# Optimization experiments

Measured on AMD Instinct MI355X. Metric: run time of the kernel, lower is better.

Reference implementation:

```python
import jax, jax.numpy as jnp
import numpy as np
from jax import lax

_CLIP_MIN = 1e-06
_CLIP_MAX = 1.0
_POS_ALPHA = 0.0005
NUM_CLASSES = 21
RADIUS = 3
HALF_D = RADIUS * RADIUS
POOL = 3
PAD = POOL // 2
IGNORE = 255
LAM = 0.5  # loss_weight_lambda, lambda_way=1


def _max_pool(x):
    # NCHW max pool, kernel=stride=3, padding=1
    return lax.reduce_window(x, -jnp.inf, lax.max,
                             (1, 1, POOL, POOL), (1, 1, POOL, POOL),
                             ((0, 0), (0, 0), (PAD, PAD), (PAD, PAD)))


def _get_pairs(x):
    # stack radius*radius shifted crops -> [N, C, r^2, nh, nw]
    h, w = x.shape[2], x.shape[3]
    nh, nw = h - RADIUS + 1, w - RADIUS + 1
    crops = [x[:, :, y:y + nh, xo:xo + nw] for y in range(RADIUS) for xo in range(RADIUS)]
    return jnp.stack(crops, axis=2)


def _log_det_by_cholesky(m):
    chol = jnp.linalg.cholesky(m)
    return 2.0 * jnp.sum(jnp.log(jnp.diagonal(chol, axis1=-2, axis2=-1) + 1e-08), axis=-1)


def _rmi_lower_bound(labels_4d, probs_4d):
    la = _max_pool(labels_4d)
    pr = _max_pool(probs_4d)
    n, c = la.shape[0], la.shape[1]
    la_v = _get_pairs(la).reshape(n, c, HALF_D, -1)   # [N,C,d,L]
    pr_v = _get_pairs(pr).reshape(n, c, HALF_D, -1)
    la_v = la_v - jnp.mean(la_v, axis=3, keepdims=True)
    pr_v = pr_v - jnp.mean(pr_v, axis=3, keepdims=True)
    la_cov = jnp.einsum('ncdl,ncel->ncde', la_v, la_v)
    pr_cov = jnp.einsum('ncdl,ncel->ncde', pr_v, pr_v)
    eye = jnp.eye(HALF_D, dtype=la_cov.dtype)
    pr_cov_inv = jnp.linalg.inv(pr_cov + eye * _POS_ALPHA)
    la_pr_cov = jnp.einsum('ncdl,ncel->ncde', la_v, pr_v)
    appro_var = la_cov - jnp.einsum('ncde,ncef,ncgf->ncdg', la_pr_cov, pr_cov_inv, la_pr_cov)
    rmi_now = 0.5 * _log_det_by_cholesky(appro_var + eye * _POS_ALPHA)  # [N,C]
    rmi_per_class = jnp.mean(rmi_now.reshape(-1, NUM_CLASSES), axis=0) / float(HALF_D)
    return jnp.sum(rmi_per_class)


def setup_inputs() -> dict:
    key = jax.random.key(0)
    k1, k2 = jax.random.split(key)
    score = jax.random.normal(k1, (4, NUM_CLASSES, 512, 512), dtype=jnp.float32)
    target = jax.random.randint(k2, (4, 512, 512), 0, NUM_CLASSES, dtype=jnp.int64)
    return {"score": score, "target": target}


def reference(score, target):
    # cross entropy with ignore_index=255, mean reduction
    logp = jax.nn.log_softmax(score, axis=1)                      # [N,C,H,W]
    valid_ce = (target != IGNORE)
    safe_t = jnp.where(valid_ce, target, 0)
    nll = -jnp.take_along_axis(logp, safe_t[:, None].astype(jnp.int32), axis=1)[:, 0]
    normal_loss = jnp.sum(jnp.where(valid_ce, nll, 0.0)) / jnp.sum(valid_ce.astype(jnp.float32))

    # valid one-hot labels and masked sigmoid probs
    mask = (target < NUM_CLASSES)                                 # [N,H,W]
    maskf = mask.astype(jnp.float32)
    onehot = jax.nn.one_hot((target * mask).astype(jnp.int32), NUM_CLASSES, dtype=jnp.float32)
    onehot = onehot * maskf[..., None]                            # [N,H,W,C]
    onehot = jnp.transpose(onehot, (0, 3, 1, 2))                  # [N,C,H,W]
    probs = jnp.clip(jax.nn.sigmoid(score) * maskf[:, None], _CLIP_MIN, _CLIP_MAX)

    rmi_loss = _rmi_lower_bound(onehot, probs)
    return LAM * normal_loss + rmi_loss * (1.0 - LAM)
```

## Files before the change

kernel.cpp:

```cpp
#include <hip/hip_runtime.h>
#include <cfloat>
#include <cmath>

#define DEVINL __device__ __forceinline__

constexpr int N_ = 4, C_ = 21, H_ = 512, W_ = 512;
constexpr int P_ = 171;
constexpr int Q_ = 169;
constexpr int NC_ = N_ * C_;
constexpr int HW_ = H_ * W_;
constexpr int PP_ = 29241;
constexpr int PROW_ = 172;
constexpr int PPAD_ = PROW_ * P_;
constexpr int NCOV_ = 189;
constexpr float EPS_ = 5e-4f;
constexpr int RC_ = 29;
constexpr int G_ = 43;

constexpr int NB_CE = N_ * HW_ / 4 / 256;
constexpr int NB_PL = (NC_ * P_ * G_ + 255) / 256;

DEVINL constexpr int tstart(int d) { return d * 9 - d * (d - 1) / 2; }

DEVINL float wave_sum(float v) {
#pragma unroll
    for (int o = 32; o > 0; o >>= 1) v += __shfl_down(v, o, 64);
    return v;
}

__global__ __launch_bounds__(256) void k_bits(const int* __restrict__ target,
                                              unsigned* __restrict__ pack) {
    int tid = blockIdx.x * 256 + threadIdx.x;
    if (tid >= N_ * PP_) return;
    int cell = tid % PP_;
    int n = tid / PP_;
    int j = cell % P_;
    int i = cell / P_;
    int hl = 3 * i - 1; if (hl < 0) hl = 0;
    int wl = 3 * j - 1; if (wl < 0) wl = 0;
    int hmax = 3 * i + 1, wmax = 3 * j + 1;
    const int* tb = target + (size_t)n * HW_;
    unsigned oh = 0, px = 0;
#pragma unroll
    for (int r = 0; r < 3; ++r) {
        int hh = hl + r;
        bool hv = hh <= hmax;
        const int* trow = tb + hh * W_;
#pragma unroll
        for (int dc = 0; dc < 3; ++dc) {
            int ww = wl + dc;
            int t = trow[ww];
            if (hv && (ww <= wmax) && t >= 0 && t < C_) {
                oh |= 1u << t;
                px |= 1u << (r * 3 + dc);
            }
        }
    }
    pack[tid] = oh | (px << 23);
}

template <int IDX>
DEVINL void do_cell(const float (&f)[3][16], unsigned pk, int c, float* prp, float* lap) {
    unsigned px = pk >> 23;
    float vm = -FLT_MAX;
#pragma unroll
    for (int r = 0; r < 3; ++r)
#pragma unroll
        for (int dc = 0; dc < 3; ++dc)
            vm = fmaxf(vm, ((px >> (r * 3 + dc)) & 1u) ? f[r][IDX + dc] : -FLT_MAX);
    float p = __builtin_amdgcn_rcpf(1.f + __expf(-vm));
    p = fminf(fmaxf(p, 1e-6f), 1.f);
    *prp = p;
    *lap = ((pk >> c) & 1u) ? 1.f : 0.f;
}

__global__ __launch_bounds__(256) void k_mix(const float* __restrict__ score,
                                             const int* __restrict__ target,
                                             const unsigned* __restrict__ pack,
                                             float* __restrict__ pr,
                                             float* __restrict__ la,
                                             float* __restrict__ cov) {
    int bid = blockIdx.x;
    int t = threadIdx.x;

    if (bid < NB_CE) {
        __shared__ float rn[4], rc[4];
        int tid = bid * 256 + t;
        int p0 = tid * 4;
        int n = p0 >> 18;
        int hw = p0 & (HW_ - 1);
        const float* sp = score + (size_t)n * C_ * HW_ + hw;
        int4 t4 = *(const int4*)(target + p0);

        float4 se = {0.f, 0.f, 0.f, 0.f};
        float4 stgt = {0.f, 0.f, 0.f, 0.f};
        float4 s[7];
#pragma unroll
        for (int cb = 0; cb < C_; cb += 7) {
#pragma unroll
            for (int u = 0; u < 7; ++u)
                s[u] = *(const float4*)(sp + (size_t)(cb + u) * HW_);
            __builtin_amdgcn_sched_barrier(0);
#pragma unroll
            for (int u = 0; u < 7; ++u) {
                int c = cb + u;
                se.x += __expf(s[u].x);
                se.y += __expf(s[u].y);
                se.z += __expf(s[u].z);
                se.w += __expf(s[u].w);
                if (t4.x == c) stgt.x = s[u].x;
                if (t4.y == c) stgt.y = s[u].y;
                if (t4.z == c) stgt.z = s[u].z;
                if (t4.w == c) stgt.w = s[u].w;
            }
        }
        float nll = 0.f, cnt = 0.f;
        if (t4.x != 255) { nll += __logf(se.x) - stgt.x; cnt += 1.f; }
        if (t4.y != 255) { nll += __logf(se.y) - stgt.y; cnt += 1.f; }
        if (t4.z != 255) { nll += __logf(se.z) - stgt.z; cnt += 1.f; }
        if (t4.w != 255) { nll += __logf(se.w) - stgt.w; cnt += 1.f; }

        nll = wave_sum(nll);
        cnt = wave_sum(cnt);
        int wv = t >> 6, lane = t & 63;
        if (lane == 0) { rn[wv] = nll; rc[wv] = cnt; }
        __syncthreads();
        if (t == 0)
            atomicAdd(&cov[NC_ * NCOV_ + 0], rn[0] + rn[1] + rn[2] + rn[3]);
        if (t == 64)
            atomicAdd(&cov[NC_ * NCOV_ + 1], rc[0] + rc[1] + rc[2] + rc[3]);
    } else {
        int tid = (bid - NB_CE) * 256 + t;
        if (tid >= NC_ * P_ * G_) return;
        int g = tid % G_;
        int rest = tid / G_;
        int i = rest % P_;
        int ncidx = rest / P_;
        int n = ncidx / C_;
        int c = ncidx - n * C_;

        int hl = 3 * i - 1; if (hl < 0) hl = 0;
        int b = (g == 0) ? 0 : 12 * g - 4;
        int o3 = (b + 15 < W_) ? 12 : 8;

        const float* sb = score + (size_t)ncidx * HW_ + (size_t)hl * W_ + b;
        float f[3][16];
#pragma unroll
        for (int r = 0; r < 3; ++r) {
            const float* rp = sb + r * W_;
            float4 q0 = *(const float4*)(rp);
            float4 q1 = *(const float4*)(rp + 4);
            float4 q2 = *(const float4*)(rp + 8);
            float4 q3 = *(const float4*)(rp + o3);
            f[r][0] = q0.x;  f[r][1] = q0.y;  f[r][2] = q0.z;  f[r][3] = q0.w;
            f[r][4] = q1.x;  f[r][5] = q1.y;  f[r][6] = q1.z;  f[r][7] = q1.w;
            f[r][8] = q2.x;  f[r][9] = q2.y;  f[r][10] = q2.z; f[r][11] = q2.w;
            f[r][12] = q3.x; f[r][13] = q3.y; f[r][14] = q3.z; f[r][15] = q3.w;
        }

        const unsigned* pkp = pack + n * PP_ + i * P_ + 4 * g;
        size_t ob = (size_t)ncidx * PPAD_ + (size_t)i * PROW_ + 4 * g;
        if (g == 0) {
            do_cell<0>(f, pkp[0], c, pr + ob + 0, la + ob + 0);
            do_cell<2>(f, pkp[1], c, pr + ob + 1, la + ob + 1);
            do_cell<5>(f, pkp[2], c, pr + ob + 2, la + ob + 2);
            do_cell<8>(f, pkp[3], c, pr + ob + 3, la + ob + 3);
        } else {
            do_cell<3>(f, pkp[0], c, pr + ob + 0, la + ob + 0);
            do_cell<6>(f, pkp[1], c, pr + ob + 1, la + ob + 1);
            do_cell<9>(f, pkp[2], c, pr + ob + 2, la + ob + 2);
            if (4 * g + 3 < P_)
                do_cell<12>(f, pkp[3], c, pr + ob + 3, la + ob + 3);
        }
    }
}

template <bool WITH_S1, int D0, int D1>
DEVINL void cov_tri(const float* __restrict__ X, float* __restrict__ cov,
                    int nc, int r0, int rend, int s1base, int s2base,
                    int tid, float (*red)[33]) {
    constexpr int NS2 = ((9 - D0) * (10 - D0) - (9 - D1) * (10 - D1)) / 2;
    constexpr int RLO = D0 / 3;
    constexpr int NS1 = WITH_S1 ? 9 : 0;
    constexpr int KOFF = tstart(D0);
    float s1[9], s2[NS2];
#pragma unroll
    for (int k = 0; k < 9; ++k) s1[k] = 0.f;
#pragma unroll
    for (int k = 0; k < NS2; ++k) s2[k] = 0.f;

    int nitems = (rend - r0) * G_;
    for (int idx = tid; idx < nitems; idx += 256) {
        int lr = idx / G_;
        int q = idx - lr * G_;
        int x0 = q * 4;
        const float* base = X + (size_t)(r0 + lr) * PROW_ + x0;
        float v[3][8];
#pragma unroll
        for (int r = RLO; r < 3; ++r) {
            float4 u0 = *(const float4*)(base + r * PROW_);
            float4 u1 = *(const float4*)(base + r * PROW_ + 4);
            v[r][0] = u0.x; v[r][1] = u0.y; v[r][2] = u0.z; v[r][3] = u0.w;
            v[r][4] = u1.x; v[r][5] = u1.y; v[r][6] = u1.z; v[r][7] = u1.w;
        }
#pragma unroll
        for (int p = 0; p < 4; ++p) {
            if (x0 + p < Q_) {
                if constexpr (WITH_S1) {
#pragma unroll
                    for (int d = 0; d < 9; ++d) s1[d] += v[d / 3][p + d % 3];
                }
                int k = 0;
#pragma unroll
                for (int d = D0; d < D1; ++d)
#pragma unroll
                    for (int e = d; e < 9; ++e) {
                        s2[k] += v[d / 3][p + d % 3] * v[e / 3][p + e % 3];
                        ++k;
                    }
            }
        }
    }

    int lane = tid & 63, wv = tid >> 6;
    if constexpr (WITH_S1) {
#pragma unroll
        for (int k = 0; k < 9; ++k) { float v2 = wave_sum(s1[k]); if (lane == 0) red[wv][k] = v2; }
    }
#pragma unroll
    for (int k = 0; k < NS2; ++k) { float v2 = wave_sum(s2[k]); if (lane == 0) red[wv][NS1 + k] = v2; }
    __syncthreads();
    for (int k = tid; k < NS1 + NS2; k += 256) {
        float v2 = red[0][k] + red[1][k] + red[2][k] + red[3][k];
        int dst = (WITH_S1 && k < 9) ? (s1base + k) : (s2base + KOFF + k - NS1);
        atomicAdd(&cov[nc * NCOV_ + dst], v2);
    }
}

template <int RA>
DEVINL void cov_ab(const float* __restrict__ A, const float* __restrict__ B,
                   float* __restrict__ cov, int nc, int r0, int rend,
                   int tid, float (*red)[33]) {
    float sab[27];
#pragma unroll
    for (int k = 0; k < 27; ++k) sab[k] = 0.f;

    int nitems = (rend - r0) * G_;
    for (int idx = tid; idx < nitems; idx += 256) {
        int lr = idx / G_;
        int q = idx - lr * G_;
        int x0 = q * 4;
        size_t off = (size_t)(r0 + lr) * PROW_ + x0;
        float a[8], b[3][8];
        {
            float4 u0 = *(const float4*)(A + off + RA * PROW_);
            float4 u1 = *(const float4*)(A + off + RA * PROW_ + 4);
            a[0] = u0.x; a[1] = u0.y; a[2] = u0.z; a[3] = u0.w;
            a[4] = u1.x; a[5] = u1.y; a[6] = u1.z; a[7] = u1.w;
        }
#pragma unroll
        for (int r = 0; r < 3; ++r) {
            float4 w0 = *(const float4*)(B + off + r * PROW_);
            float4 w1 = *(const float4*)(B + off + r * PROW_ + 4);
            b[r][0] = w0.x; b[r][1] = w0.y; b[r][2] = w0.z; b[r][3] = w0.w;
            b[r][4] = w1.x; b[r][5] = w1.y; b[r][6] = w1.z; b[r][7] = w1.w;
        }
#pragma unroll
        for (int p = 0; p < 4; ++p) {
            if (x0 + p < Q_) {
#pragma unroll
                for (int dm = 0; dm < 3; ++dm)
#pragma unroll
                    for (int e = 0; e < 9; ++e)
                        sab[dm * 9 + e] += a[p + dm] * b[e / 3][p + e % 3];
            }
        }
    }

    int lane = tid & 63, wv = tid >> 6;
#pragma unroll
    for (int k = 0; k < 27; ++k) { float v2 = wave_sum(sab[k]); if (lane == 0) red[wv][k] = v2; }
    __syncthreads();
    for (int k = tid; k < 27; k += 256) {
        float v2 = red[0][k] + red[1][k] + red[2][k] + red[3][k];
        atomicAdd(&cov[nc * NCOV_ + 108 + RA * 27 + k], v2);
    }
}

__global__ __launch_bounds__(256) void k_cov(const float* __restrict__ la,
                                             const float* __restrict__ pr,
                                             float* __restrict__ cov) {
    __shared__ float red[4][33];
    int nc = blockIdx.x;
    int chunk = blockIdx.y;
    int part = blockIdx.z;
    int r0 = chunk * RC_;
    int rend = r0 + RC_;
    if (rend > Q_) rend = Q_;
    int tid = threadIdx.x;
    const float* LA = la + (size_t)nc * PPAD_;
    const float* PR = pr + (size_t)nc * PPAD_;

    switch (part) {
        case 0: cov_tri<true, 0, 3>(LA, cov, nc, r0, rend, 0, 18, tid, red); break;
        case 1: cov_tri<false, 3, 9>(LA, cov, nc, r0, rend, 0, 18, tid, red); break;
        case 2: cov_tri<true, 0, 3>(PR, cov, nc, r0, rend, 9, 63, tid, red); break;
        case 3: cov_tri<false, 3, 9>(PR, cov, nc, r0, rend, 9, 63, tid, red); break;
        case 4: cov_ab<0>(LA, PR, cov, nc, r0, rend, tid, red); break;
        case 5: cov_ab<1>(LA, PR, cov, nc, r0, rend, tid, red); break;
        case 6: cov_ab<2>(LA, PR, cov, nc, r0, rend, tid, red); break;
    }
}

__global__ __launch_bounds__(128) void k_final(const float* __restrict__ cov,
                                               float* __restrict__ out) {
    __shared__ float red[128];
    int t = threadIdx.x;
    float my = 0.f;
    if (t < NC_) {
        const float* S = cov + t * NCOV_;
        const float Lf = (float)(Q_ * Q_);
        float sA[9], sB[9];
#pragma unroll
        for (int d = 0; d < 9; ++d) { sA[d] = S[d]; sB[d] = S[9 + d]; }
        float laC[45], M[45], Cm[81];
        {
            int k = 0;
#pragma unroll
            for (int d = 0; d < 9; ++d)
#pragma unroll
                for (int e = d; e < 9; ++e) {
                    laC[k] = S[18 + k] - sA[d] * sA[e] / Lf;
                    M[k] = S[63 + k] - sB[d] * sB[e] / Lf + (d == e ? EPS_ : 0.f);
                    ++k;
                }
#pragma unroll
            for (int d = 0; d < 9; ++d)
#pragma unroll
                for (int e = 0; e < 9; ++e)
                    Cm[d * 9 + e] = S[108 + d * 9 + e] - sA[d] * sB[e] / Lf;
        }
#pragma unroll
        for (int j = 0; j < 9; ++j) {
            float s = M[tstart(j)];
#pragma unroll
            for (int k = 0; k < j; ++k) { float l = M[tstart(k) + (j - k)]; s -= l * l; }
            float dj = sqrtf(fmaxf(s, 1e-30f));
            M[tstart(j)] = dj;
            float inv = 1.f / dj;
#pragma unroll
            for (int i = j + 1; i < 9; ++i) {
                float s2 = M[tstart(j) + (i - j)];
#pragma unroll
                for (int k = 0; k < j; ++k)
                    s2 -= M[tstart(k) + (i - k)] * M[tstart(k) + (j - k)];
                M[tstart(j) + (i - j)] = s2 * inv;
            }
        }
#pragma unroll
        for (int p = 0; p < 9; ++p) {
#pragma unroll
            for (int i = 0; i < 9; ++i) {
                float s = Cm[p * 9 + i];
#pragma unroll
                for (int k = 0; k < i; ++k)
                    s -= M[tstart(k) + (i - k)] * Cm[p * 9 + k];
                Cm[p * 9 + i] = s / M[tstart(i)];
            }
        }
#pragma unroll
        for (int d = 0; d < 9; ++d)
#pragma unroll
            for (int e = d; e < 9; ++e) {
                float s = 0.f;
#pragma unroll
                for (int i = 0; i < 9; ++i) s += Cm[d * 9 + i] * Cm[e * 9 + i];
                laC[tstart(d) + (e - d)] -= s;
                if (d == e) laC[tstart(d)] += EPS_;
            }
        float rmi = 0.f;
#pragma unroll
        for (int j = 0; j < 9; ++j) {
            float s = laC[tstart(j)];
#pragma unroll
            for (int k = 0; k < j; ++k) { float l = laC[tstart(k) + (j - k)]; s -= l * l; }
            float dj = sqrtf(fmaxf(s, 0.f));
            laC[tstart(j)] = dj;
            float inv = 1.f / fmaxf(dj, 1e-30f);
#pragma unroll
            for (int i = j + 1; i < 9; ++i) {
                float s2 = laC[tstart(j) + (i - j)];
#pragma unroll
                for (int k = 0; k < j; ++k)
                    s2 -= laC[tstart(k) + (i - k)] * laC[tstart(k) + (j - k)];
                laC[tstart(j) + (i - j)] = s2 * inv;
            }
            rmi += __logf(dj + 1e-8f);
        }
        my = rmi;
    }
    red[t] = my;
    __syncthreads();
#pragma unroll
    for (int o = 64; o > 0; o >>= 1) {
        if (t < o) red[t] += red[t + o];
        __syncthreads();
    }
    if (t == 0) {
        float rmi_total = red[0] / 36.f;
        float ce = cov[NC_ * NCOV_ + 0] / cov[NC_ * NCOV_ + 1];
        out[0] = 0.5f * ce + 0.5f * rmi_total;
    }
}

extern "C" void kernel_launch(void* const* d_in, const int* in_sizes, int n_in,
                              void* d_out, int out_size, void* d_ws, size_t ws_size,
                              hipStream_t stream) {
    const float* score = (const float*)d_in[0];
    const int* target = (const int*)d_in[1];
    float* pr = (float*)d_ws;
    float* la = pr + (size_t)NC_ * PPAD_;
    float* cov = la + (size_t)NC_ * PPAD_;
    unsigned* pack = (unsigned*)(cov + NC_ * NCOV_ + 2);
    hipMemsetAsync(cov, 0, (size_t)(NC_ * NCOV_ + 2) * sizeof(float), stream);

    k_bits<<<dim3((N_ * PP_ + 255) / 256), dim3(256), 0, stream>>>(target, pack);
    k_mix<<<dim3(NB_CE + NB_PL), dim3(256), 0, stream>>>(score, target, pack, pr, la, cov);
    k_cov<<<dim3(NC_, 6, 7), dim3(256), 0, stream>>>(la, pr, cov);
    k_final<<<dim3(1), dim3(128), 0, stream>>>(cov, (float*)d_out);
}
```

Baseline: 244.0 us.

## Stage covariance row window in LDS and compute all covariance parts per block

The covariance kernel used to launch seven separate blocks per (nc, chunk), each reading the same la/pr rows from global memory. Now one block per (nc, chunk) loads a 31-row window of la and pr into shared memory once, then runs both full triangular covariances and the three cross-covariance stages from LDS in sequence. This cuts redundant global reads and the launch to 504 blocks, at the cost of fewer blocks (lower parallelism) and more registers, since a full 45-entry triangle is now accumulated per thread. It also swaps a sched_barrier in the CE path for an empty asm register fence to pin the loads before use.

New measurement: 268.1 us. 9.9% more time.

```diff
diff --git a/kernel.cpp b/kernel.cpp
--- a/kernel.cpp
+++ b/kernel.cpp
@@ -16,9 +16,12 @@
 constexpr float EPS_ = 5e-4f;
 constexpr int RC_ = 29;
 constexpr int G_ = 43;
+constexpr int NWINMAX_ = 31;
 
 constexpr int NB_CE = N_ * HW_ / 4 / 256;
 constexpr int NB_PL = (NC_ * P_ * G_ + 255) / 256;
+
+typedef float f4_t __attribute__((ext_vector_type(4)));
 
 DEVINL constexpr int tstart(int d) { return d * 9 - d * (d - 1) / 2; }
 
@@ -94,13 +97,14 @@
 
         float4 se = {0.f, 0.f, 0.f, 0.f};
         float4 stgt = {0.f, 0.f, 0.f, 0.f};
-        float4 s[7];
+        f4_t s[7];
 #pragma unroll
         for (int cb = 0; cb < C_; cb += 7) {
 #pragma unroll
             for (int u = 0; u < 7; ++u)
-                s[u] = *(const float4*)(sp + (size_t)(cb + u) * HW_);
-            __builtin_amdgcn_sched_barrier(0);
+                s[u] = *(const f4_t*)(sp + (size_t)(cb + u) * HW_);
+            asm volatile("" : "+v"(s[0]), "+v"(s[1]), "+v"(s[2]), "+v"(s[3]),
+                              "+v"(s[4]), "+v"(s[5]), "+v"(s[6]));
 #pragma unroll
             for (int u = 0; u < 7; ++u) {
                 int c = cb + u;
@@ -175,29 +179,24 @@
     }
 }
 
-template <bool WITH_S1, int D0, int D1>
-DEVINL void cov_tri(const float* __restrict__ X, float* __restrict__ cov,
-                    int nc, int r0, int rend, int s1base, int s2base,
-                    int tid, float (*red)[33]) {
-    constexpr int NS2 = ((9 - D0) * (10 - D0) - (9 - D1) * (10 - D1)) / 2;
-    constexpr int RLO = D0 / 3;
-    constexpr int NS1 = WITH_S1 ? 9 : 0;
-    constexpr int KOFF = tstart(D0);
-    float s1[9], s2[NS2];
+DEVINL void stage_tri(const float* __restrict__ X, float* __restrict__ cov,
+                      int nc, int nrows, int s1base, int s2base,
+                      int tid, float (*red)[54]) {
+    float s1[9], s2[45];
 #pragma unroll
     for (int k = 0; k < 9; ++k) s1[k] = 0.f;
 #pragma unroll
-    for (int k = 0; k < NS2; ++k) s2[k] = 0.f;
-
-    int nitems = (rend - r0) * G_;
+    for (int k = 0; k < 45; ++k) s2[k] = 0.f;
+
+    int nitems = nrows * G_;
     for (int idx = tid; idx < nitems; idx += 256) {
         int lr = idx / G_;
         int q = idx - lr * G_;
         int x0 = q * 4;
-        const float* base = X + (size_t)(r0 + lr) * PROW_ + x0;
+        const float* base = X + lr * PROW_ + x0;
         float v[3][8];
 #pragma unroll
-        for (int r = RLO; r < 3; ++r) {
+        for (int r = 0; r < 3; ++r) {
             float4 u0 = *(const float4*)(base + r * PROW_);
             float4 u1 = *(const float4*)(base + r * PROW_ + 4);
             v[r][0] = u0.x; v[r][1] = u0.y; v[r][2] = u0.z; v[r][3] = u0.w;
@@ -206,13 +205,11 @@
 #pragma unroll
         for (int p = 0; p < 4; ++p) {
             if (x0 + p < Q_) {
-                if constexpr (WITH_S1) {
-#pragma unroll
-                    for (int d = 0; d < 9; ++d) s1[d] += v[d / 3][p + d % 3];
-                }
+#pragma unroll
+                for (int d = 0; d < 9; ++d) s1[d] += v[d / 3][p + d % 3];
                 int k = 0;
 #pragma unroll
-                for (int d = D0; d < D1; ++d)
+                for (int d = 0; d < 9; ++d)
 #pragma unroll
                     for (int e = d; e < 9; ++e) {
                         s2[k] += v[d / 3][p + d % 3] * v[e / 3][p + e % 3];
@@ -223,45 +220,45 @@
     }
 
     int lane = tid & 63, wv = tid >> 6;
-    if constexpr (WITH_S1) {
-#pragma unroll
-        for (int k = 0; k < 9; ++k) { float v2 = wave_sum(s1[k]); if (lane == 0) red[wv][k] = v2; }
-    }
-#pragma unroll
-    for (int k = 0; k < NS2; ++k) { float v2 = wave_sum(s2[k]); if (lane == 0) red[wv][NS1 + k] = v2; }
-    __syncthreads();
-    for (int k = tid; k < NS1 + NS2; k += 256) {
-        float v2 = red[0][k] + red[1][k] + red[2][k] + red[3][k];
-        int dst = (WITH_S1 && k < 9) ? (s1base + k) : (s2base + KOFF + k - NS1);
+#pragma unroll
+    for (int k = 0; k < 9; ++k) { float v2 = wave_sum(s1[k]); if (lane == 0) red[wv][k] = v2; }
+#pragma unroll
+    for (int k = 0; k < 45; ++k) { float v2 = wave_sum(s2[k]); if (lane == 0) red[wv][9 + k] = v2; }
+    __syncthreads();
+    if (tid < 54) {
+        float v2 = red[0][tid] + red[1][tid] + red[2][tid] + red[3][tid];
+        int dst = (tid < 9) ? (s1base + tid) : (s2base + tid - 9);
         atomicAdd(&cov[nc * NCOV_ + dst], v2);
     }
+    __syncthreads();
 }
 
 template <int RA>
-DEVINL void cov_ab(const float* __restrict__ A, const float* __restrict__ B,
-                   float* __restrict__ cov, int nc, int r0, int rend,
-                   int tid, float (*red)[33]) {
+DEVINL void stage_ab(const float* __restrict__ XA, const float* __restrict__ XB,
+                     float* __restrict__ cov, int nc, int nrows,
+                     int tid, float (*red)[54]) {
     float sab[27];
 #pragma unroll
     for (int k = 0; k < 27; ++k) sab[k] = 0.f;
 
-    int nitems = (rend - r0) * G_;
+    int nitems = nrows * G_;
     for (int idx = tid; idx < nitems; idx += 256) {
         int lr = idx / G_;
         int q = idx - lr * G_;
         int x0 = q * 4;
-        size_t off = (size_t)(r0 + lr) * PROW_ + x0;
         float a[8], b[3][8];
         {
-            float4 u0 = *(const float4*)(A + off + RA * PROW_);
-            float4 u1 = *(const float4*)(A + off + RA * PROW_ + 4);
+            const float* pa = XA + (lr + RA) * PROW_ + x0;
+            float4 u0 = *(const float4*)(pa);
+            float4 u1 = *(const float4*)(pa + 4);
             a[0] = u0.x; a[1] = u0.y; a[2] = u0.z; a[3] = u0.w;
             a[4] = u1.x; a[5] = u1.y; a[6] = u1.z; a[7] = u1.w;
         }
+        const float* pb = XB + lr * PROW_ + x0;
 #pragma unroll
         for (int r = 0; r < 3; ++r) {
-            float4 w0 = *(const float4*)(B + off + r * PROW_);
-            float4 w1 = *(const float4*)(B + off + r * PROW_ + 4);
+            float4 w0 = *(const float4*)(pb + r * PROW_);
+            float4 w1 = *(const float4*)(pb + r * PROW_ + 4);
             b[r][0] = w0.x; b[r][1] = w0.y; b[r][2] = w0.z; b[r][3] = w0.w;
             b[r][4] = w1.x; b[r][5] = w1.y; b[r][6] = w1.z; b[r][7] = w1.w;
         }
@@ -281,35 +278,42 @@
 #pragma unroll
     for (int k = 0; k < 27; ++k) { float v2 = wave_sum(sab[k]); if (lane == 0) red[wv][k] = v2; }
     __syncthreads();
-    for (int k = tid; k < 27; k += 256) {
-        float v2 = red[0][k] + red[1][k] + red[2][k] + red[3][k];
-        atomicAdd(&cov[nc * NCOV_ + 108 + RA * 27 + k], v2);
-    }
+    if (tid < 27) {
+        float v2 = red[0][tid] + red[1][tid] + red[2][tid] + red[3][tid];
+        atomicAdd(&cov[nc * NCOV_ + 108 + RA * 27 + tid], v2);
+    }
+    __syncthreads();
 }
 
 __global__ __launch_bounds__(256) void k_cov(const float* __restrict__ la,
                                              const float* __restrict__ pr,
                                              float* __restrict__ cov) {
-    __shared__ float red[4][33];
+    __shared__ float ldsA[NWINMAX_ * PROW_ + 8];
+    __shared__ float ldsB[NWINMAX_ * PROW_ + 8];
+    __shared__ float red[4][54];
     int nc = blockIdx.x;
     int chunk = blockIdx.y;
-    int part = blockIdx.z;
     int r0 = chunk * RC_;
     int rend = r0 + RC_;
     if (rend > Q_) rend = Q_;
+    int nrows = rend - r0;
+    int nwin = nrows + 2;
     int tid = threadIdx.x;
-    const float* LA = la + (size_t)nc * PPAD_;
-    const float* PR = pr + (size_t)nc * PPAD_;
-
-    switch (part) {
-        case 0: cov_tri<true, 0, 3>(LA, cov, nc, r0, rend, 0, 18, tid, red); break;
-        case 1: cov_tri<false, 3, 9>(LA, cov, nc, r0, rend, 0, 18, tid, red); break;
-        case 2: cov_tri<true, 0, 3>(PR, cov, nc, r0, rend, 9, 63, tid, red); break;
-        case 3: cov_tri<false, 3, 9>(PR, cov, nc, r0, rend, 9, 63, tid, red); break;
-        case 4: cov_ab<0>(LA, PR, cov, nc, r0, rend, tid, red); break;
-        case 5: cov_ab<1>(LA, PR, cov, nc, r0, rend, tid, red); break;
-        case 6: cov_ab<2>(LA, PR, cov, nc, r0, rend, tid, red); break;
-    }
+
+    const float* LA = la + (size_t)nc * PPAD_ + (size_t)r0 * PROW_;
+    const float* PR = pr + (size_t)nc * PPAD_ + (size_t)r0 * PROW_;
+    int nq = nwin * G_;
+    for (int idx = tid; idx < nq; idx += 256) {
+        *(float4*)(ldsA + idx * 4) = *(const float4*)(LA + idx * 4);
+        *(float4*)(ldsB + idx * 4) = *(const float4*)(PR + idx * 4);
+    }
+    __syncthreads();
+
+    stage_tri(ldsA, cov, nc, nrows, 0, 18, tid, red);
+    stage_tri(ldsB, cov, nc, nrows, 9, 63, tid, red);
+    stage_ab<0>(ldsA, ldsB, cov, nc, nrows, tid, red);
+    stage_ab<1>(ldsA, ldsB, cov, nc, nrows, tid, red);
+    stage_ab<2>(ldsA, ldsB, cov, nc, nrows, tid, red);
 }
 
 __global__ __launch_bounds__(128) void k_final(const float* __restrict__ cov,
@@ -426,6 +430,6 @@
 
     k_bits<<<dim3((N_ * PP_ + 255) / 256), dim3(256), 0, stream>>>(target, pack);
     k_mix<<<dim3(NB_CE + NB_PL), dim3(256), 0, stream>>>(score, target, pack, pr, la, cov);
-    k_cov<<<dim3(NC_, 6, 7), dim3(256), 0, stream>>>(la, pr, cov);
+    k_cov<<<dim3(NC_, 6), dim3(256), 0, stream>>>(la, pr, cov);
     k_final<<<dim3(1), dim3(128), 0, stream>>>(cov, (float*)d_out);
 }
```

## Split first-moment sums into separate cov part, use DPP wave reductions

Applied to the files above, without the earlier changes.

Moves the first-moment (mean) sums for both label and prob maps out of the triangular covariance parts into a new eighth k_cov part. It also enlarges the row chunk so the grid becomes 4x8 instead of 6x7 per class. Warp reductions now use DPP row shifts and broadcasts, with lane 63 holding the result, instead of shuffle-down. The cross-term loop is restructured to load one B row at a time to cut register pressure, and the CE loads use an empty asm barrier in place of sched_barrier. Together these aim to lower register use, reduction latency and per-block imbalance, at the cost of fewer, larger blocks and an extra pass that reads both maps.

Measured after the change: 254.2 us. 1.04x slower.

```diff
diff --git a/kernel.cpp b/kernel.cpp
--- a/kernel.cpp
+++ b/kernel.cpp
@@ -14,17 +14,29 @@
 constexpr int PPAD_ = PROW_ * P_;
 constexpr int NCOV_ = 189;
 constexpr float EPS_ = 5e-4f;
-constexpr int RC_ = 29;
+constexpr int RC_ = 43;
 constexpr int G_ = 43;
 
 constexpr int NB_CE = N_ * HW_ / 4 / 256;
 constexpr int NB_PL = (NC_ * P_ * G_ + 255) / 256;
 
+typedef float f4_t __attribute__((ext_vector_type(4)));
+
 DEVINL constexpr int tstart(int d) { return d * 9 - d * (d - 1) / 2; }
 
-DEVINL float wave_sum(float v) {
-#pragma unroll
-    for (int o = 32; o > 0; o >>= 1) v += __shfl_down(v, o, 64);
+template <int CTRL>
+DEVINL float dpp_add(float v) {
+    int x = __builtin_amdgcn_update_dpp(0, __float_as_int(v), CTRL, 0xF, 0xF, false);
+    return v + __int_as_float(x);
+}
+
+DEVINL float wave_sum63(float v) {
+    v = dpp_add<0x111>(v);
+    v = dpp_add<0x112>(v);
+    v = dpp_add<0x114>(v);
+    v = dpp_add<0x118>(v);
+    v = dpp_add<0x142>(v);
+    v = dpp_add<0x143>(v);
     return v;
 }
 
@@ -94,13 +106,14 @@
 
         float4 se = {0.f, 0.f, 0.f, 0.f};
         float4 stgt = {0.f, 0.f, 0.f, 0.f};
-        float4 s[7];
+        f4_t s[7];
 #pragma unroll
         for (int cb = 0; cb < C_; cb += 7) {
 #pragma unroll
             for (int u = 0; u < 7; ++u)
-                s[u] = *(const float4*)(sp + (size_t)(cb + u) * HW_);
-            __builtin_amdgcn_sched_barrier(0);
+                s[u] = *(const f4_t*)(sp + (size_t)(cb + u) * HW_);
+            asm volatile("" : "+v"(s[0]), "+v"(s[1]), "+v"(s[2]), "+v"(s[3]),
+                              "+v"(s[4]), "+v"(s[5]), "+v"(s[6]));
 #pragma unroll
             for (int u = 0; u < 7; ++u) {
                 int c = cb + u;
@@ -120,10 +133,10 @@
         if (t4.z != 255) { nll += __logf(se.z) - stgt.z; cnt += 1.f; }
         if (t4.w != 255) { nll += __logf(se.w) - stgt.w; cnt += 1.f; }
 
-        nll = wave_sum(nll);
-        cnt = wave_sum(cnt);
+        nll = wave_sum63(nll);
+        cnt = wave_sum63(cnt);
         int wv = t >> 6, lane = t & 63;
-        if (lane == 0) { rn[wv] = nll; rc[wv] = cnt; }
+        if (lane == 63) { rn[wv] = nll; rc[wv] = cnt; }
         __syncthreads();
         if (t == 0)
             atomicAdd(&cov[NC_ * NCOV_ + 0], rn[0] + rn[1] + rn[2] + rn[3]);
@@ -175,17 +188,14 @@
     }
 }
 
-template <bool WITH_S1, int D0, int D1>
+template <int D0, int D1>
 DEVINL void cov_tri(const float* __restrict__ X, float* __restrict__ cov,
-                    int nc, int r0, int rend, int s1base, int s2base,
-                    int tid, float (*red)[33]) {
+                    int nc, int r0, int rend, int s2base,
+                    int tid, float (*red)[27]) {
     constexpr int NS2 = ((9 - D0) * (10 - D0) - (9 - D1) * (10 - D1)) / 2;
     constexpr int RLO = D0 / 3;
-    constexpr int NS1 = WITH_S1 ? 9 : 0;
     constexpr int KOFF = tstart(D0);
-    float s1[9], s2[NS2];
-#pragma unroll
-    for (int k = 0; k < 9; ++k) s1[k] = 0.f;
+    float s2[NS2];
 #pragma unroll
     for (int k = 0; k < NS2; ++k) s2[k] = 0.f;
 
@@ -206,10 +216,6 @@
 #pragma unroll
         for (int p = 0; p < 4; ++p) {
             if (x0 + p < Q_) {
-                if constexpr (WITH_S1) {
-#pragma unroll
-                    for (int d = 0; d < 9; ++d) s1[d] += v[d / 3][p + d % 3];
-                }
                 int k = 0;
 #pragma unroll
                 for (int d = D0; d < D1; ++d)
@@ -223,24 +229,22 @@
     }
 
     int lane = tid & 63, wv = tid >> 6;
-    if constexpr (WITH_S1) {
-#pragma unroll
-        for (int k = 0; k < 9; ++k) { float v2 = wave_sum(s1[k]); if (lane == 0) red[wv][k] = v2; }
-    }
-#pragma unroll
-    for (int k = 0; k < NS2; ++k) { float v2 = wave_sum(s2[k]); if (lane == 0) red[wv][NS1 + k] = v2; }
+#pragma unroll
+    for (int k = 0; k < NS2; ++k) {
+        float v2 = wave_sum63(s2[k]);
+        if (lane == 63) red[wv][k] = v2;
+    }
     __syncthreads();
-    for (int k = tid; k < NS1 + NS2; k += 256) {
-        float v2 = red[0][k] + red[1][k] + red[2][k] + red[3][k];
-        int dst = (WITH_S1 && k < 9) ? (s1base + k) : (s2base + KOFF + k - NS1);
-        atomicAdd(&cov[nc * NCOV_ + dst], v2);
+    if (tid < NS2) {
+        float v2 = red[0][tid] + red[1][tid] + red[2][tid] + red[3][tid];
+        atomicAdd(&cov[nc * NCOV_ + s2base + KOFF + tid], v2);
     }
 }
 
 template <int RA>
 DEVINL void cov_ab(const float* __restrict__ A, const float* __restrict__ B,
                    float* __restrict__ cov, int nc, int r0, int rend,
-                   int tid, float (*red)[33]) {
+                   int tid, float (*red)[27]) {
     float sab[27];
 #pragma unroll
     for (int k = 0; k < 27; ++k) sab[k] = 0.f;
@@ -251,7 +255,7 @@
         int q = idx - lr * G_;
         int x0 = q * 4;
         size_t off = (size_t)(r0 + lr) * PROW_ + x0;
-        float a[8], b[3][8];
+        float a[8];
         {
             float4 u0 = *(const float4*)(A + off + RA * PROW_);
             float4 u1 = *(const float4*)(A + off + RA * PROW_ + 4);
@@ -260,37 +264,100 @@
         }
 #pragma unroll
         for (int r = 0; r < 3; ++r) {
-            float4 w0 = *(const float4*)(B + off + r * PROW_);
-            float4 w1 = *(const float4*)(B + off + r * PROW_ + 4);
-            b[r][0] = w0.x; b[r][1] = w0.y; b[r][2] = w0.z; b[r][3] = w0.w;
-            b[r][4] = w1.x; b[r][5] = w1.y; b[r][6] = w1.z; b[r][7] = w1.w;
-        }
-#pragma unroll
-        for (int p = 0; p < 4; ++p) {
-            if (x0 + p < Q_) {
-#pragma unroll
-                for (int dm = 0; dm < 3; ++dm)
-#pragma unroll
-                    for (int e = 0; e < 9; ++e)
-                        sab[dm * 9 + e] += a[p + dm] * b[e / 3][p + e % 3];
+            float b[8];
+            {
+                float4 w0 = *(const float4*)(B + off + r * PROW_);
+                float4 w1 = *(const float4*)(B + off + r * PROW_ + 4);
+                b[0] = w0.x; b[1] = w0.y; b[2] = w0.z; b[3] = w0.w;
+                b[4] = w1.x; b[5] = w1.y; b[6] = w1.z; b[7] = w1.w;
+            }
+#pragma unroll
+            for (int p = 0; p < 4; ++p) {
+                if (x0 + p < Q_) {
+#pragma unroll
+                    for (int dm = 0; dm < 3; ++dm)
+#pragma unroll
+                        for (int e2 = 0; e2 < 3; ++e2)
+                            sab[dm * 9 + r * 3 + e2] += a[p + dm] * b[p + e2];
+                }
             }
         }
     }
 
     int lane = tid & 63, wv = tid >> 6;
 #pragma unroll
-    for (int k = 0; k < 27; ++k) { float v2 = wave_sum(sab[k]); if (lane == 0) red[wv][k] = v2; }
+    for (int k = 0; k < 27; ++k) {
+        float v2 = wave_sum63(sab[k]);
+        if (lane == 63) red[wv][k] = v2;
+    }
     __syncthreads();
-    for (int k = tid; k < 27; k += 256) {
-        float v2 = red[0][k] + red[1][k] + red[2][k] + red[3][k];
-        atomicAdd(&cov[nc * NCOV_ + 108 + RA * 27 + k], v2);
+    if (tid < 27) {
+        float v2 = red[0][tid] + red[1][tid] + red[2][tid] + red[3][tid];
+        atomicAdd(&cov[nc * NCOV_ + 108 + RA * 27 + tid], v2);
+    }
+}
+
+DEVINL void cov_s1(const float* __restrict__ LA, const float* __restrict__ PR,
+                   float* __restrict__ cov, int nc, int r0, int rend,
+                   int tid, float (*red)[27]) {
+    float s1a[9], s1b[9];
+#pragma unroll
+    for (int k = 0; k < 9; ++k) { s1a[k] = 0.f; s1b[k] = 0.f; }
+
+    int nitems = (rend - r0) * G_;
+    for (int idx = tid; idx < nitems; idx += 256) {
+        int lr = idx / G_;
+        int q = idx - lr * G_;
+        int x0 = q * 4;
+        size_t off = (size_t)(r0 + lr) * PROW_ + x0;
+#pragma unroll
+        for (int r = 0; r < 3; ++r) {
+            float va[8], vb[8];
+            {
+                float4 u0 = *(const float4*)(LA + off + r * PROW_);
+                float4 u1 = *(const float4*)(LA + off + r * PROW_ + 4);
+                va[0] = u0.x; va[1] = u0.y; va[2] = u0.z; va[3] = u0.w;
+                va[4] = u1.x; va[5] = u1.y; va[6] = u1.z; va[7] = u1.w;
+                float4 w0 = *(const float4*)(PR + off + r * PROW_);
+                float4 w1 = *(const float4*)(PR + off + r * PROW_ + 4);
+                vb[0] = w0.x; vb[1] = w0.y; vb[2] = w0.z; vb[3] = w0.w;
+                vb[4] = w1.x; vb[5] = w1.y; vb[6] = w1.z; vb[7] = w1.w;
+            }
+#pragma unroll
+            for (int p = 0; p < 4; ++p) {
+                if (x0 + p < Q_) {
+#pragma unroll
+                    for (int dc = 0; dc < 3; ++dc) {
+                        s1a[r * 3 + dc] += va[p + dc];
+                        s1b[r * 3 + dc] += vb[p + dc];
+                    }
+                }
+            }
+        }
+    }
+
+    int lane = tid & 63, wv = tid >> 6;
+#pragma unroll
+    for (int k = 0; k < 9; ++k) {
+        float v2 = wave_sum63(s1a[k]);
+        if (lane == 63) red[wv][k] = v2;
+    }
+#pragma unroll
+    for (int k = 0; k < 9; ++k) {
+        float v2 = wave_sum63(s1b[k]);
+        if (lane == 63) red[wv][9 + k] = v2;
+    }
+    __syncthreads();
+    if (tid < 18) {
+        float v2 = red[0][tid] + red[1][tid] + red[2][tid] + red[3][tid];
+        atomicAdd(&cov[nc * NCOV_ + tid], v2);
     }
 }
 
 __global__ __launch_bounds__(256) void k_cov(const float* __restrict__ la,
                                              const float* __restrict__ pr,
                                              float* __restrict__ cov) {
-    __shared__ float red[4][33];
+    __shared__ float red[4][27];
     int nc = blockIdx.x;
     int chunk = blockIdx.y;
     int part = blockIdx.z;
@@ -302,13 +369,14 @@
     const float* PR = pr + (size_t)nc * PPAD_;
 
     switch (part) {
-        case 0: cov_tri<true, 0, 3>(LA, cov, nc, r0, rend, 0, 18, tid, red); break;
-        case 1: cov_tri<false, 3, 9>(LA, cov, nc, r0, rend, 0, 18, tid, red); break;
-        case 2: cov_tri<true, 0, 3>(PR, cov, nc, r0, rend, 9, 63, tid, red); break;
-        case 3: cov_tri<false, 3, 9>(PR, cov, nc, r0, rend, 9, 63, tid, red); break;
+        case 0: cov_tri<0, 3>(LA, cov, nc, r0, rend, 18, tid, red); break;
+        case 1: cov_tri<3, 9>(LA, cov, nc, r0, rend, 18, tid, red); break;
+        case 2: cov_tri<0, 3>(PR, cov, nc, r0, rend, 63, tid, red); break;
+        case 3: cov_tri<3, 9>(PR, cov, nc, r0, rend, 63, tid, red); break;
         case 4: cov_ab<0>(LA, PR, cov, nc, r0, rend, tid, red); break;
         case 5: cov_ab<1>(LA, PR, cov, nc, r0, rend, tid, red); break;
         case 6: cov_ab<2>(LA, PR, cov, nc, r0, rend, tid, red); break;
+        case 7: cov_s1(LA, PR, cov, nc, r0, rend, tid, red); break;
     }
 }
 
@@ -426,6 +494,6 @@
 
     k_bits<<<dim3((N_ * PP_ + 255) / 256), dim3(256), 0, stream>>>(target, pack);
     k_mix<<<dim3(NB_CE + NB_PL), dim3(256), 0, stream>>>(score, target, pack, pr, la, cov);
-    k_cov<<<dim3(NC_, 6, 7), dim3(256), 0, stream>>>(la, pr, cov);
+    k_cov<<<dim3(NC_, 4, 8), dim3(256), 0, stream>>>(la, pr, cov);
     k_final<<<dim3(1), dim3(128), 0, stream>>>(cov, (float*)d_out);
 }
```
